# Kernel tuning notes

Hardware: AMD Instinct MI355X
Metric: run time of the kernel (lower is better)

The kernel has to match this reference:

```python
import jax, jax.numpy as jnp
import numpy as np

V, D, H, L, F, MAXLEN = 30522, 768, 12, 12, 3072, 1000
B, S = 16, 512
DH = D // H
SCALE = np.float32(1.0 / np.sqrt(DH))


def setup_inputs() -> dict:
    key = jax.random.key(0)
    ks = jax.random.split(key, 32)
    p = lambda k, shape: (jax.random.normal(k, shape, dtype=jnp.float32) * 0.02)
    inp = {}
    inp["tokens"] = jax.random.randint(ks[0], (B, S), 0, V, dtype=jnp.int32)
    inp["segments"] = jax.random.randint(ks[1], (B, S), 0, 2, dtype=jnp.int32)
    inp["valid_lens"] = jax.random.randint(ks[2], (B,), 64, S + 1, dtype=jnp.int32)
    inp["tok_emb"] = p(ks[3], (V, D))
    inp["seg_emb"] = p(ks[4], (2, D))
    inp["pos_emb"] = jax.random.normal(ks[5], (1, MAXLEN, D), dtype=jnp.float32)
    # stacked per-layer parameters (L leading axis); Linear stored as [in,out]
    inp["Wq"] = p(ks[6], (L, D, D)); inp["bq"] = p(ks[7], (L, D))
    inp["Wk"] = p(ks[8], (L, D, D)); inp["bk"] = p(ks[9], (L, D))
    inp["Wv"] = p(ks[10], (L, D, D)); inp["bv"] = p(ks[11], (L, D))
    inp["Wo"] = p(ks[12], (L, D, D)); inp["bo"] = p(ks[13], (L, D))
    inp["W1"] = p(ks[14], (L, D, F)); inp["b1"] = p(ks[15], (L, F))
    inp["W2"] = p(ks[16], (L, F, D)); inp["b2"] = p(ks[17], (L, D))
    inp["ln1_g"] = jnp.ones((L, D), jnp.float32); inp["ln1_b"] = jnp.zeros((L, D), jnp.float32)
    inp["ln2_g"] = jnp.ones((L, D), jnp.float32); inp["ln2_b"] = jnp.zeros((L, D), jnp.float32)
    return inp


def _layer_norm(x, g, b):
    m = jnp.mean(x, axis=-1, keepdims=True)
    v = jnp.var(x, axis=-1, keepdims=True)
    return (x - m) * jax.lax.rsqrt(v + 1e-5) * g + b


def reference(tokens, segments, valid_lens, tok_emb, seg_emb, pos_emb,
              Wq, bq, Wk, bk, Wv, bv, Wo, bo, W1, b1, W2, b2,
              ln1_g, ln1_b, ln2_g, ln2_b):
    # embeddings + positional add (pos_embedding.data -> no grad, matched via stop_gradient)
    X = tok_emb[tokens] + seg_emb[segments] + jax.lax.stop_gradient(pos_emb)[:, :S, :]
    # key positions >= valid_len are masked (fill -1e6, like the torch code)
    key_mask = jnp.arange(S)[None, :] >= valid_lens[:, None]  # [B,S]

    def blk(X, params):
        wq, bq_, wk, bk_, wv, bv_, wo, bo_, w1, b1_, w2, b2_, g1, be1, g2, be2 = params
        heads = lambda y: y.reshape(B, S, H, DH).transpose(0, 2, 1, 3)  # [B,H,S,DH]
        q = heads(X @ wq + bq_)
        k = heads(X @ wk + bk_)
        v = heads(X @ wv + bv_)
        scores = jnp.einsum('bhqd,bhkd->bhqk', q, k) * SCALE  # [B,H,S,S]
        scores = jnp.where(key_mask[:, None, None, :], jnp.float32(-1e6), scores)
        w = jax.nn.softmax(scores, axis=-1)
        o = jnp.einsum('bhqk,bhkd->bhqd', w, v).transpose(0, 2, 1, 3).reshape(B, S, D)
        X = _layer_norm(X + o @ wo + bo_, g1, be1)
        Y = jax.nn.relu(X @ w1 + b1_) @ w2 + b2_
        X = _layer_norm(X + Y, g2, be2)
        return X, None

    params = (Wq, bq, Wk, bk, Wv, bv, Wo, bo, W1, b1, W2, b2, ln1_g, ln1_b, ln2_g, ln2_b)
    X, _ = jax.lax.scan(blk, X, params)
    return X
```

## Files before the change

### kernel.cpp

```cpp
#include <hip/hip_runtime.h>
#include <hip/hip_bf16.h>

typedef __bf16 bf16_t;
typedef __bf16 bf16x8 __attribute__((ext_vector_type(8)));
typedef float  f32x4  __attribute__((ext_vector_type(4)));

static constexpr int ND = 768;
static constexpr int NH = 12;
static constexpr int NL = 12;
static constexpr int NF = 3072;
static constexpr int NB = 16;
static constexpr int NS = 512;
static constexpr int DH = 64;
static constexpr int MTOK = NB * NS;

#define MFMA_BF16 __builtin_amdgcn_mfma_f32_16x16x32_bf16

__device__ __forceinline__ void gload16(const bf16_t* g, const bf16_t* l) {
    __builtin_amdgcn_global_load_lds(
        (const __attribute__((address_space(1))) void*)(unsigned long long)g,
        (__attribute__((address_space(3))) void*)(unsigned int)(unsigned long long)l,
        16, 0, 0);
}

__global__ __launch_bounds__(256) void embed_kernel(
    const int* __restrict__ tokens, const int* __restrict__ segments,
    const float* __restrict__ tok_emb, const float* __restrict__ seg_emb,
    const float* __restrict__ pos_emb, float* __restrict__ X,
    bf16_t* __restrict__ Xb)
{
    const int t = blockIdx.x;
    const int s = t & (NS - 1);
    const int tok = tokens[t], seg = segments[t];
    const float* te = tok_emb + (size_t)tok * ND;
    const float* se = seg_emb + (size_t)seg * ND;
    const float* pe = pos_emb + (size_t)s * ND;
#pragma unroll
    for (int i = 0; i < 3; ++i) {
        int d = threadIdx.x + i * 256;
        float v = te[d] + se[d] + pe[d];
        X[(size_t)t * ND + d]  = v;
        Xb[(size_t)t * ND + d] = (bf16_t)v;
    }
}

__global__ __launch_bounds__(256) void transpose_kernel(
    const float* __restrict__ src, bf16_t* __restrict__ dst,
    int K, int N, size_t src_stride, size_t dst_stride)
{
    __shared__ float tile[32][33];
    const float* s = src + blockIdx.z * src_stride;
    bf16_t*      d = dst + blockIdx.z * dst_stride;
    const int n0 = blockIdx.x * 32, k0 = blockIdx.y * 32;
#pragma unroll
    for (int i = threadIdx.y; i < 32; i += 8)
        tile[i][threadIdx.x] = s[(size_t)(k0 + i) * N + n0 + threadIdx.x];
    __syncthreads();
#pragma unroll
    for (int i = threadIdx.y; i < 32; i += 8)
        d[(size_t)(n0 + i) * K + k0 + threadIdx.x] = (bf16_t)tile[threadIdx.x][i];
}

__global__ __launch_bounds__(256) void concat_bias_kernel(
    const float* __restrict__ bq, const float* __restrict__ bk,
    const float* __restrict__ bv, float* __restrict__ fb)
{
    int idx = blockIdx.x * 256 + threadIdx.x;
    if (idx >= NL * 2304) return;
    int l = idx / 2304, c = idx % 2304;
    float v = (c < 768) ? bq[l * 768 + c]
            : (c < 1536) ? bk[l * 768 + c - 768] : bv[l * 768 + c - 1536];
    fb[idx] = v;
}

template <int MODE>
__global__ __launch_bounds__(256) void gemm_v3(
    const bf16_t* __restrict__ A, const bf16_t* __restrict__ Bt,
    const float* __restrict__ bias, const float* __restrict__ resid,
    float* __restrict__ outF, bf16_t* __restrict__ o1,
    bf16_t* __restrict__ o2, bf16_t* __restrict__ o3,
    int K, int N, int gridN)
{
    __shared__ __align__(16) bf16_t As[2][128 * 64];
    __shared__ __align__(16) bf16_t Bs[2][128 * 64];
    const int nwg = gridDim.x;
    const int l2 = (blockIdx.x & 7) * (nwg >> 3) + (blockIdx.x >> 3);
    const int m0 = (l2 / gridN) * 128, n0 = (l2 % gridN) * 128;

    const int tid = threadIdx.x, lane = tid & 63, wid = tid >> 6;
    const int wr = (wid >> 1) * 64, wc = (wid & 1) * 64;
    const int fr = lane & 15, g = lane >> 4;
    const int sr = lane >> 3;
    const int ssw = ((lane & 7) ^ sr) * 8;

    f32x4 acc[4][4] = {};
    const int nk = K >> 6;

    auto stage = [&](int buf, int kt) {
        const int k0 = kt << 6;
#pragma unroll
        for (int i = 0; i < 4; ++i) {
            const int lr = wid * 32 + i * 8;
            gload16(A + (size_t)(m0 + lr + sr) * K + k0 + ssw, &As[buf][lr * 64]);
        }
#pragma unroll
        for (int i = 0; i < 4; ++i) {
            const int lr = wid * 32 + i * 8;
            gload16(Bt + (size_t)(n0 + lr + sr) * K + k0 + ssw, &Bs[buf][lr * 64]);
        }
    };

    stage(0, 0);
    for (int kt = 0; kt < nk; ++kt) {
        const int cur = kt & 1;
        if (kt + 1 < nk) {
            stage(cur ^ 1, kt + 1);
            asm volatile("s_waitcnt vmcnt(8)" ::: "memory");
        } else {
            asm volatile("s_waitcnt vmcnt(0)" ::: "memory");
        }
        __builtin_amdgcn_s_barrier();
        asm volatile("" ::: "memory");
#pragma unroll
        for (int kk = 0; kk < 2; ++kk) {
            bf16x8 af[4], bfv[4];
#pragma unroll
            for (int m = 0; m < 4; ++m) {
                const int row = wr + m * 16 + fr;
                af[m] = *(const bf16x8*)(
                    &As[cur][row * 64 + (((kk * 4 + g) ^ (fr & 7)) * 8)]);
            }
#pragma unroll
            for (int n = 0; n < 4; ++n) {
                const int row = wc + n * 16 + fr;
                bfv[n] = *(const bf16x8*)(
                    &Bs[cur][row * 64 + (((kk * 4 + g) ^ (fr & 7)) * 8)]);
            }
            __builtin_amdgcn_s_setprio(1);
#pragma unroll
            for (int m = 0; m < 4; ++m)
#pragma unroll
                for (int n = 0; n < 4; ++n)
                    acc[m][n] = MFMA_BF16(af[m], bfv[n], acc[m][n], 0, 0, 0);
            __builtin_amdgcn_s_setprio(0);
        }
        asm volatile("" ::: "memory");
        __builtin_amdgcn_s_barrier();
    }

    const int rr = (lane >> 4) * 4, cc = lane & 15;
#pragma unroll
    for (int m = 0; m < 4; ++m)
#pragma unroll
        for (int n = 0; n < 4; ++n)
#pragma unroll
            for (int j = 0; j < 4; ++j) {
                const int row = m0 + wr + m * 16 + rr + j;
                const int col = n0 + wc + n * 16 + cc;
                const float v = acc[m][n][j] + bias[col];
                if constexpr (MODE == 2) {
                    const size_t idx = (size_t)row * N + col;
                    outF[idx] = v + resid[idx];
                } else if constexpr (MODE == 3) {
                    o1[(size_t)row * N + col] = (bf16_t)fmaxf(v, 0.0f);
                } else {
                    if (col < 768) {
                        o1[(size_t)row * 768 + col] = (bf16_t)v;
                    } else if (col < 1536) {
                        o2[(size_t)row * 768 + col - 768] = (bf16_t)v;
                    } else {
                        const int c = col - 1536;
                        const int b = row >> 9, s = row & (NS - 1);
                        const int hh = c >> 6, dh = c & (DH - 1);
                        o3[(((size_t)(b * NH + hh)) * DH + dh) * NS + s] = (bf16_t)v;
                    }
                }
            }
}

__global__ __launch_bounds__(256) void attn_kernel(
    const bf16_t* __restrict__ Q, const bf16_t* __restrict__ K,
    const bf16_t* __restrict__ Vt, const int* __restrict__ vlens,
    bf16_t* __restrict__ O)
{
    const int h = blockIdx.x, b = blockIdx.y, qb = blockIdx.z;
    const int wid = threadIdx.x >> 6, lane = threadIdx.x & 63;
    const int q0 = qb * 128 + wid * 32;
    const int vl = vlens[b];
    const int fr = lane & 15, g = lane >> 4, g8 = g * 8;

    __shared__ __align__(16) bf16_t Ks[2][64 * 64];
    __shared__ __align__(16) bf16_t Vs[2][64 * 64];
    __shared__ __align__(16) bf16_t Plds[4][32 * 72];
    bf16_t* pl = Plds[wid];

    const bf16_t* kbase = K + ((size_t)(b * NS) * ND + h * DH);
    const bf16_t* vbase = Vt + ((size_t)(b * NH + h) * DH) * NS;

    bf16x8 qf[2][2];
#pragma unroll
    for (int qg = 0; qg < 2; ++qg) {
        const bf16_t* qptr = Q + ((size_t)(b * NS + q0 + qg * 16 + fr) * ND + h * DH);
        qf[qg][0] = *(const bf16x8*)(qptr + g8);
        qf[qg][1] = *(const bf16x8*)(qptr + 32 + g8);
    }
    asm volatile("s_waitcnt vmcnt(0)" ::: "memory");

    f32x4 acc_o[2][4] = {};
    float mrow[2][4], lrow[2][4];
#pragma unroll
    for (int qg = 0; qg < 2; ++qg)
#pragma unroll
        for (int j = 0; j < 4; ++j) { mrow[qg][j] = -1e30f; lrow[qg][j] = 0.f; }

    auto stage = [&](int buf, int t) {
        const int kv0 = t * 64;
#pragma unroll
        for (int i = 0; i < 2; ++i) {
            const int lr = wid * 16 + i * 8;
            const int r  = lr + (lane >> 3);
            const int ss = ((lane & 7) ^ (r & 7)) * 8;
            gload16(kbase + (size_t)(kv0 + r) * ND + ss, &Ks[buf][lr * 64]);
            gload16(vbase + (size_t)r * NS + kv0 + ss,   &Vs[buf][lr * 64]);
        }
    };

    stage(0, 0);
    for (int t = 0; t < 8; ++t) {
        const int cur = t & 1;
        const int kv0 = t * 64;
        if (t < 7) {
            stage(cur ^ 1, t + 1);
            asm volatile("s_waitcnt vmcnt(4)" ::: "memory");
        } else {
            asm volatile("s_waitcnt vmcnt(0)" ::: "memory");
        }
        __builtin_amdgcn_s_barrier();
        asm volatile("" ::: "memory");

        const bf16_t* ks = Ks[cur];
        const bf16_t* vs = Vs[cur];

        f32x4 sc[2][4];
#pragma unroll
        for (int qg = 0; qg < 2; ++qg)
#pragma unroll
            for (int f = 0; f < 4; ++f) sc[qg][f] = (f32x4){0.f, 0.f, 0.f, 0.f};
#pragma unroll
        for (int f = 0; f < 4; ++f) {
            const int row = f * 16 + fr;
            const bf16_t* kr = ks + row * 64;
            bf16x8 kf0 = *(const bf16x8*)(kr + ((g ^ (row & 7)) * 8));
            bf16x8 kf1 = *(const bf16x8*)(kr + (((g + 4) ^ (row & 7)) * 8));
            sc[0][f] = MFMA_BF16(qf[0][0], kf0, sc[0][f], 0, 0, 0);
            sc[0][f] = MFMA_BF16(qf[0][1], kf1, sc[0][f], 0, 0, 0);
            sc[1][f] = MFMA_BF16(qf[1][0], kf0, sc[1][f], 0, 0, 0);
            sc[1][f] = MFMA_BF16(qf[1][1], kf1, sc[1][f], 0, 0, 0);
        }

#pragma unroll
        for (int qg = 0; qg < 2; ++qg) {
            float sv[16];
#pragma unroll
            for (int f = 0; f < 4; ++f) {
                const int col = kv0 + f * 16 + fr;
                const bool masked = col >= vl;
#pragma unroll
                for (int j = 0; j < 4; ++j)
                    sv[f * 4 + j] = masked ? -1e6f : sc[qg][f][j] * 0.125f;
            }
            float pm[4], rs[4], scl[4];
#pragma unroll
            for (int j = 0; j < 4; ++j)
                pm[j] = fmaxf(fmaxf(sv[j], sv[4 + j]), fmaxf(sv[8 + j], sv[12 + j]));
#pragma unroll
            for (int msk = 1; msk < 16; msk <<= 1)
#pragma unroll
                for (int j = 0; j < 4; ++j) pm[j] = fmaxf(pm[j], __shfl_xor(pm[j], msk));
#pragma unroll
            for (int j = 0; j < 4; ++j) {
                const float mnew = fmaxf(mrow[qg][j], pm[j]);
                scl[j] = __expf(mrow[qg][j] - mnew);
                mrow[qg][j] = mnew;
                rs[j] = 0.f;
            }
#pragma unroll
            for (int f = 0; f < 4; ++f)
#pragma unroll
                for (int j = 0; j < 4; ++j) {
                    const float pv = __expf(sv[f * 4 + j] - mrow[qg][j]);
                    rs[j] += pv;
                    pl[(qg * 16 + g * 4 + j) * 72 + f * 16 + fr] = (bf16_t)pv;
                }
#pragma unroll
            for (int msk = 1; msk < 16; msk <<= 1)
#pragma unroll
                for (int j = 0; j < 4; ++j) rs[j] += __shfl_xor(rs[j], msk);
#pragma unroll
            for (int j = 0; j < 4; ++j) {
                lrow[qg][j] = lrow[qg][j] * scl[j] + rs[j];
#pragma unroll
                for (int n = 0; n < 4; ++n) acc_o[qg][n][j] *= scl[j];
            }
        }

        bf16x8 pf[2][2];
#pragma unroll
        for (int qg = 0; qg < 2; ++qg)
#pragma unroll
            for (int c = 0; c < 2; ++c)
                pf[qg][c] = *(const bf16x8*)(pl + (qg * 16 + fr) * 72 + c * 32 + g8);
#pragma unroll
        for (int n = 0; n < 4; ++n) {
            const int row = n * 16 + fr;
            const bf16_t* vr = vs + row * 64;
            bf16x8 vf0 = *(const bf16x8*)(vr + ((g ^ (row & 7)) * 8));
            bf16x8 vf1 = *(const bf16x8*)(vr + (((g + 4) ^ (row & 7)) * 8));
            acc_o[0][n] = MFMA_BF16(pf[0][0], vf0, acc_o[0][n], 0, 0, 0);
            acc_o[0][n] = MFMA_BF16(pf[0][1], vf1, acc_o[0][n], 0, 0, 0);
            acc_o[1][n] = MFMA_BF16(pf[1][0], vf0, acc_o[1][n], 0, 0, 0);
            acc_o[1][n] = MFMA_BF16(pf[1][1], vf1, acc_o[1][n], 0, 0, 0);
        }

        asm volatile("" ::: "memory");
        __builtin_amdgcn_s_barrier();
    }

#pragma unroll
    for (int qg = 0; qg < 2; ++qg)
#pragma unroll
        for (int n = 0; n < 4; ++n)
#pragma unroll
            for (int j = 0; j < 4; ++j) {
                const int row = q0 + qg * 16 + g * 4 + j;
                O[(size_t)(b * NS + row) * ND + h * DH + n * 16 + fr] =
                    (bf16_t)(acc_o[qg][n][j] / lrow[qg][j]);
            }
}

__global__ __launch_bounds__(256) void ln_kernel(
    const float* __restrict__ Z, const float* __restrict__ g,
    const float* __restrict__ bt, float* __restrict__ X, bf16_t* __restrict__ Xb)
{
    const int t = blockIdx.x;
    const float* z = Z + (size_t)t * ND;
    float x[3];
#pragma unroll
    for (int i = 0; i < 3; ++i) x[i] = z[threadIdx.x + i * 256];
    float s = x[0] + x[1] + x[2];
    float ss = x[0] * x[0] + x[1] * x[1] + x[2] * x[2];
#pragma unroll
    for (int m = 1; m < 64; m <<= 1) {
        s += __shfl_xor(s, m);
        ss += __shfl_xor(ss, m);
    }
    __shared__ float red[8];
    const int wid = threadIdx.x >> 6, lane = threadIdx.x & 63;
    if (lane == 0) { red[wid] = s; red[4 + wid] = ss; }
    __syncthreads();
    s = red[0] + red[1] + red[2] + red[3];
    ss = red[4] + red[5] + red[6] + red[7];
    const float mean = s * (1.0f / ND);
    const float var = ss * (1.0f / ND) - mean * mean;
    const float inv = rsqrtf(var + 1e-5f);
#pragma unroll
    for (int i = 0; i < 3; ++i) {
        int d = threadIdx.x + i * 256;
        float y = (x[i] - mean) * inv * g[d] + bt[d];
        X[(size_t)t * ND + d] = y;
        Xb[(size_t)t * ND + d] = (bf16_t)y;
    }
}

extern "C" void kernel_launch(void* const* d_in, const int* in_sizes, int n_in,
                              void* d_out, int out_size, void* d_ws, size_t ws_size,
                              hipStream_t stream)
{
    (void)in_sizes; (void)n_in; (void)out_size; (void)ws_size;
    const int*   tokens   = (const int*)d_in[0];
    const int*   segments = (const int*)d_in[1];
    const int*   vlens    = (const int*)d_in[2];
    const float* tok_emb  = (const float*)d_in[3];
    const float* seg_emb  = (const float*)d_in[4];
    const float* pos_emb  = (const float*)d_in[5];
    const float* Wq = (const float*)d_in[6];  const float* bq = (const float*)d_in[7];
    const float* Wk = (const float*)d_in[8];  const float* bk = (const float*)d_in[9];
    const float* Wv = (const float*)d_in[10]; const float* bv = (const float*)d_in[11];
    const float* Wo = (const float*)d_in[12]; const float* bo = (const float*)d_in[13];
    const float* W1 = (const float*)d_in[14]; const float* b1 = (const float*)d_in[15];
    const float* W2 = (const float*)d_in[16]; const float* b2 = (const float*)d_in[17];
    const float* g1 = (const float*)d_in[18]; const float* be1 = (const float*)d_in[19];
    const float* g2 = (const float*)d_in[20]; const float* be2 = (const float*)d_in[21];

    float* X = (float*)d_out;

    char* p = (char*)d_ws;
    auto carve = [&](size_t elems, size_t esz) {
        void* r = (void*)p;
        p += (elems * esz + 255) & ~(size_t)255;
        return r;
    };
    bf16_t* wqkvT = (bf16_t*)carve((size_t)NL * 2304 * ND, 2);
    bf16_t* woT   = (bf16_t*)carve((size_t)NL * ND * ND, 2);
    bf16_t* w1T   = (bf16_t*)carve((size_t)NL * NF * ND, 2);
    bf16_t* w2T   = (bf16_t*)carve((size_t)NL * ND * NF, 2);
    float*  fb    = (float*)carve((size_t)NL * 2304, 4);
    bf16_t* Xb    = (bf16_t*)carve((size_t)MTOK * ND, 2);
    bf16_t* Qb    = (bf16_t*)carve((size_t)MTOK * ND, 2);
    bf16_t* Kb    = (bf16_t*)carve((size_t)MTOK * ND, 2);
    bf16_t* Vtb   = (bf16_t*)carve((size_t)MTOK * ND, 2);
    bf16_t* Ob    = (bf16_t*)carve((size_t)MTOK * ND, 2);
    bf16_t* H1    = (bf16_t*)carve((size_t)MTOK * NF, 2);
    float*  Z     = (float*)carve((size_t)MTOK * ND, 4);

    embed_kernel<<<MTOK, 256, 0, stream>>>(tokens, segments, tok_emb, seg_emb,
                                           pos_emb, X, Xb);
    const dim3 tb(32, 8);
    const size_t qkvs = (size_t)2304 * ND;
    transpose_kernel<<<dim3(ND / 32, ND / 32, NL), tb, 0, stream>>>(
        Wq, wqkvT, ND, ND, (size_t)ND * ND, qkvs);
    transpose_kernel<<<dim3(ND / 32, ND / 32, NL), tb, 0, stream>>>(
        Wk, wqkvT + (size_t)768 * ND, ND, ND, (size_t)ND * ND, qkvs);
    transpose_kernel<<<dim3(ND / 32, ND / 32, NL), tb, 0, stream>>>(
        Wv, wqkvT + (size_t)1536 * ND, ND, ND, (size_t)ND * ND, qkvs);
    transpose_kernel<<<dim3(ND / 32, ND / 32, NL), tb, 0, stream>>>(
        Wo, woT, ND, ND, (size_t)ND * ND, (size_t)ND * ND);
    transpose_kernel<<<dim3(NF / 32, ND / 32, NL), tb, 0, stream>>>(
        W1, w1T, ND, NF, (size_t)ND * NF, (size_t)NF * ND);
    transpose_kernel<<<dim3(ND / 32, NF / 32, NL), tb, 0, stream>>>(
        W2, w2T, NF, ND, (size_t)NF * ND, (size_t)ND * NF);
    concat_bias_kernel<<<(NL * 2304 + 255) / 256, 256, 0, stream>>>(bq, bk, bv, fb);

    for (int l = 0; l < NL; ++l) {
        gemm_v3<4><<<18 * 64, 256, 0, stream>>>(
            Xb, wqkvT + (size_t)l * qkvs, fb + (size_t)l * 2304,
            nullptr, nullptr, Qb, Kb, Vtb, ND, 2304, 18);
        attn_kernel<<<dim3(NH, NB, NS / 128), 256, 0, stream>>>(Qb, Kb, Vtb, vlens, Ob);
        gemm_v3<2><<<6 * 64, 256, 0, stream>>>(
            Ob, woT + (size_t)l * ND * ND, bo + l * ND, X, Z,
            nullptr, nullptr, nullptr, ND, ND, 6);
        ln_kernel<<<MTOK, 256, 0, stream>>>(Z, g1 + l * ND, be1 + l * ND, X, Xb);
        gemm_v3<3><<<24 * 64, 256, 0, stream>>>(
            Xb, w1T + (size_t)l * ND * NF, b1 + l * NF, nullptr, nullptr,
            H1, nullptr, nullptr, ND, NF, 24);
        gemm_v3<2><<<6 * 64, 256, 0, stream>>>(
            H1, w2T + (size_t)l * ND * NF, b2 + l * ND, X, Z,
            nullptr, nullptr, nullptr, NF, ND, 6);
        ln_kernel<<<MTOK, 256, 0, stream>>>(Z, g2 + l * ND, be2 + l * ND, X, Xb);
    }
}
```

Baseline: 3.132 ms.

## Use 256x256-tile 8-wave GEMM with phased prefetch for QKV and FFN1

Adds a gemm256 kernel that uses 512 threads (8 waves) and 256x256 output tiles, with each wave computing 128x64. Global-to-LDS prefetch of the next K-tile is split across four sub-phases and interleaved with MFMA work, using per-phase barriers. The aim is more data reuse per LDS byte and better overlap of loads with compute for the QKV and FFN-up GEMMs. The cost is higher register pressure (a 32-fragment accumulator), 128KB of LDS per block, and fewer blocks (288 and 384) in flight on the many CUs. The N=768 GEMMs keep the old 128x128 kernel, now specialized to the residual-output mode.

```diff
diff --git a/kernel.cpp b/kernel.cpp
--- a/kernel.cpp
+++ b/kernel.cpp
@@ -15,6 +15,7 @@
 static constexpr int MTOK = NB * NS;
 
 #define MFMA_BF16 __builtin_amdgcn_mfma_f32_16x16x32_bf16
+#define FENCE() asm volatile("" ::: "memory")
 
 __device__ __forceinline__ void gload16(const bf16_t* g, const bf16_t* l) {
     __builtin_amdgcn_global_load_lds(
@@ -74,94 +75,101 @@
 }
 
 template <int MODE>
-__global__ __launch_bounds__(256) void gemm_v3(
+__global__ __launch_bounds__(512, 2) void gemm256(
     const bf16_t* __restrict__ A, const bf16_t* __restrict__ Bt,
-    const float* __restrict__ bias, const float* __restrict__ resid,
-    float* __restrict__ outF, bf16_t* __restrict__ o1,
-    bf16_t* __restrict__ o2, bf16_t* __restrict__ o3,
+    const float* __restrict__ bias,
+    bf16_t* __restrict__ o1, bf16_t* __restrict__ o2, bf16_t* __restrict__ o3,
     int K, int N, int gridN)
 {
-    __shared__ __align__(16) bf16_t As[2][128 * 64];
-    __shared__ __align__(16) bf16_t Bs[2][128 * 64];
+    __shared__ __align__(16) bf16_t As[2][2][128 * 64];
+    __shared__ __align__(16) bf16_t Bs[2][2][128 * 64];
     const int nwg = gridDim.x;
     const int l2 = (blockIdx.x & 7) * (nwg >> 3) + (blockIdx.x >> 3);
-    const int m0 = (l2 / gridN) * 128, n0 = (l2 % gridN) * 128;
-
+    const int m0 = (l2 / gridN) * 256, n0 = (l2 % gridN) * 256;
     const int tid = threadIdx.x, lane = tid & 63, wid = tid >> 6;
-    const int wr = (wid >> 1) * 64, wc = (wid & 1) * 64;
+    const int wm = wid >> 2, wn = wid & 3;
     const int fr = lane & 15, g = lane >> 4;
-    const int sr = lane >> 3;
-    const int ssw = ((lane & 7) ^ sr) * 8;
-
-    f32x4 acc[4][4] = {};
-    const int nk = K >> 6;
-
-    auto stage = [&](int buf, int kt) {
-        const int k0 = kt << 6;
-#pragma unroll
-        for (int i = 0; i < 4; ++i) {
-            const int lr = wid * 32 + i * 8;
-            gload16(A + (size_t)(m0 + lr + sr) * K + k0 + ssw, &As[buf][lr * 64]);
-        }
-#pragma unroll
-        for (int i = 0; i < 4; ++i) {
-            const int lr = wid * 32 + i * 8;
-            gload16(Bt + (size_t)(n0 + lr + sr) * K + k0 + ssw, &Bs[buf][lr * 64]);
-        }
+    const int sr8 = lane >> 3, sc = lane & 7;
+    const int nt = K >> 6;
+
+    auto stA = [&](int buf, int half, int j, int kt) {
+        const int r = j * 64 + wid * 8 + sr8;
+        gload16(A + (size_t)(m0 + half * 128 + r) * K + (kt << 6) + ((sc ^ sr8) * 8),
+                &As[buf][half][j * 4096 + wid * 512]);
     };
-
-    stage(0, 0);
-    for (int kt = 0; kt < nk; ++kt) {
-        const int cur = kt & 1;
-        if (kt + 1 < nk) {
-            stage(cur ^ 1, kt + 1);
-            asm volatile("s_waitcnt vmcnt(8)" ::: "memory");
-        } else {
-            asm volatile("s_waitcnt vmcnt(0)" ::: "memory");
-        }
-        __builtin_amdgcn_s_barrier();
-        asm volatile("" ::: "memory");
-#pragma unroll
-        for (int kk = 0; kk < 2; ++kk) {
-            bf16x8 af[4], bfv[4];
-#pragma unroll
-            for (int m = 0; m < 4; ++m) {
-                const int row = wr + m * 16 + fr;
-                af[m] = *(const bf16x8*)(
-                    &As[cur][row * 64 + (((kk * 4 + g) ^ (fr & 7)) * 8)]);
-            }
-#pragma unroll
-            for (int n = 0; n < 4; ++n) {
-                const int row = wc + n * 16 + fr;
-                bfv[n] = *(const bf16x8*)(
-                    &Bs[cur][row * 64 + (((kk * 4 + g) ^ (fr & 7)) * 8)]);
-            }
+    auto stB = [&](int buf, int half, int j, int kt) {
+        const int r = j * 64 + wid * 8 + sr8;
+        gload16(Bt + (size_t)(n0 + half * 128 + r) * K + (kt << 6) + ((sc ^ sr8) * 8),
+                &Bs[buf][half][j * 4096 + wid * 512]);
+    };
+
+    stB(0, 0, 0, 0); stB(0, 0, 1, 0); stB(0, 1, 0, 0); stB(0, 1, 1, 0);
+    stA(0, 0, 0, 0); stA(0, 1, 0, 0); stA(0, 0, 1, 0); stA(0, 1, 1, 0);
+    asm volatile("s_waitcnt vmcnt(0)" ::: "memory");
+    FENCE(); __builtin_amdgcn_s_barrier(); FENCE();
+
+    f32x4 acc[8][4] = {};
+    for (int t = 0; t < nt; ++t) {
+        const int buf = t & 1, nb = buf ^ 1;
+        const bf16_t* Ah = &As[buf][wm][0];
+        const bf16_t* Bh = &Bs[buf][wn >> 1][0];
+        const int brow = (wn & 1) * 64;
+        const bool pf = (t + 1 < nt);
+
+        bf16x8 bfr[4][2];
+#pragma unroll
+        for (int nf = 0; nf < 4; ++nf)
+#pragma unroll
+            for (int ks = 0; ks < 2; ++ks)
+                bfr[nf][ks] = *(const bf16x8*)&Bh[(brow + nf * 16 + fr) * 64 +
+                                                  (((ks * 4 + g) ^ (fr & 7)) * 8)];
+#pragma unroll
+        for (int p = 0; p < 4; ++p) {
+            bf16x8 afr[2][2];
+#pragma unroll
+            for (int i = 0; i < 2; ++i)
+#pragma unroll
+                for (int ks = 0; ks < 2; ++ks)
+                    afr[i][ks] = *(const bf16x8*)&Ah[((p * 2 + i) * 16 + fr) * 64 +
+                                                     (((ks * 4 + g) ^ (fr & 7)) * 8)];
+            if (pf) {
+                if (p == 0)      { stB(nb, 0, 0, t + 1); stB(nb, 0, 1, t + 1); }
+                else if (p == 1) { stB(nb, 1, 0, t + 1); stB(nb, 1, 1, t + 1); }
+                else if (p == 2) { stA(nb, 0, 0, t + 1); stA(nb, 1, 0, t + 1); }
+                else             { stA(nb, 0, 1, t + 1); stA(nb, 1, 1, t + 1); }
+            }
+            if (p == 1) {
+                if (pf) asm volatile("s_waitcnt vmcnt(4)" ::: "memory");
+                else    asm volatile("s_waitcnt vmcnt(0)" ::: "memory");
+            }
+            if (p == 3 && pf) asm volatile("s_waitcnt vmcnt(2)" ::: "memory");
+            FENCE(); __builtin_amdgcn_s_barrier(); FENCE();
+            asm volatile("s_waitcnt lgkmcnt(0)" ::: "memory");
             __builtin_amdgcn_s_setprio(1);
 #pragma unroll
-            for (int m = 0; m < 4; ++m)
-#pragma unroll
-                for (int n = 0; n < 4; ++n)
-                    acc[m][n] = MFMA_BF16(af[m], bfv[n], acc[m][n], 0, 0, 0);
+            for (int i = 0; i < 2; ++i)
+#pragma unroll
+                for (int nf = 0; nf < 4; ++nf)
+#pragma unroll
+                    for (int ks = 0; ks < 2; ++ks)
+                        acc[p * 2 + i][nf] =
+                            MFMA_BF16(afr[i][ks], bfr[nf][ks], acc[p * 2 + i][nf], 0, 0, 0);
             __builtin_amdgcn_s_setprio(0);
-        }
-        asm volatile("" ::: "memory");
-        __builtin_amdgcn_s_barrier();
+            FENCE(); __builtin_amdgcn_s_barrier(); FENCE();
+        }
     }
 
     const int rr = (lane >> 4) * 4, cc = lane & 15;
 #pragma unroll
-    for (int m = 0; m < 4; ++m)
-#pragma unroll
-        for (int n = 0; n < 4; ++n)
+    for (int mf = 0; mf < 8; ++mf)
+#pragma unroll
+        for (int nf = 0; nf < 4; ++nf)
 #pragma unroll
             for (int j = 0; j < 4; ++j) {
-                const int row = m0 + wr + m * 16 + rr + j;
-                const int col = n0 + wc + n * 16 + cc;
-                const float v = acc[m][n][j] + bias[col];
-                if constexpr (MODE == 2) {
-                    const size_t idx = (size_t)row * N + col;
-                    outF[idx] = v + resid[idx];
-                } else if constexpr (MODE == 3) {
+                const int row = m0 + wm * 128 + mf * 16 + rr + j;
+                const int col = n0 + wn * 64 + nf * 16 + cc;
+                const float v = acc[mf][nf][j] + bias[col];
+                if constexpr (MODE == 3) {
                     o1[(size_t)row * N + col] = (bf16_t)fmaxf(v, 0.0f);
                 } else {
                     if (col < 768) {
@@ -178,6 +186,92 @@
             }
 }
 
+template <int MODE>
+__global__ __launch_bounds__(256) void gemm_v3(
+    const bf16_t* __restrict__ A, const bf16_t* __restrict__ Bt,
+    const float* __restrict__ bias, const float* __restrict__ resid,
+    float* __restrict__ outF, int K, int N, int gridN)
+{
+    __shared__ __align__(16) bf16_t As[2][128 * 64];
+    __shared__ __align__(16) bf16_t Bs[2][128 * 64];
+    const int nwg = gridDim.x;
+    const int l2 = (blockIdx.x & 7) * (nwg >> 3) + (blockIdx.x >> 3);
+    const int m0 = (l2 / gridN) * 128, n0 = (l2 % gridN) * 128;
+
+    const int tid = threadIdx.x, lane = tid & 63, wid = tid >> 6;
+    const int wr = (wid >> 1) * 64, wc = (wid & 1) * 64;
+    const int fr = lane & 15, g = lane >> 4;
+    const int sr = lane >> 3;
+    const int ssw = ((lane & 7) ^ sr) * 8;
+
+    f32x4 acc[4][4] = {};
+    const int nk = K >> 6;
+
+    auto stage = [&](int buf, int kt) {
+        const int k0 = kt << 6;
+#pragma unroll
+        for (int i = 0; i < 4; ++i) {
+            const int lr = wid * 32 + i * 8;
+            gload16(A + (size_t)(m0 + lr + sr) * K + k0 + ssw, &As[buf][lr * 64]);
+        }
+#pragma unroll
+        for (int i = 0; i < 4; ++i) {
+            const int lr = wid * 32 + i * 8;
+            gload16(Bt + (size_t)(n0 + lr + sr) * K + k0 + ssw, &Bs[buf][lr * 64]);
+        }
+    };
+
+    stage(0, 0);
+    for (int kt = 0; kt < nk; ++kt) {
+        const int cur = kt & 1;
+        if (kt + 1 < nk) {
+            stage(cur ^ 1, kt + 1);
+            asm volatile("s_waitcnt vmcnt(8)" ::: "memory");
+        } else {
+            asm volatile("s_waitcnt vmcnt(0)" ::: "memory");
+        }
+        FENCE(); __builtin_amdgcn_s_barrier(); FENCE();
+#pragma unroll
+        for (int kk = 0; kk < 2; ++kk) {
+            bf16x8 af[4], bfv[4];
+#pragma unroll
+            for (int m = 0; m < 4; ++m) {
+                const int row = wr + m * 16 + fr;
+                af[m] = *(const bf16x8*)(
+                    &As[cur][row * 64 + (((kk * 4 + g) ^ (fr & 7)) * 8)]);
+            }
+#pragma unroll
+            for (int n = 0; n < 4; ++n) {
+                const int row = wc + n * 16 + fr;
+                bfv[n] = *(const bf16x8*)(
+                    &Bs[cur][row * 64 + (((kk * 4 + g) ^ (fr & 7)) * 8)]);
+            }
+            __builtin_amdgcn_s_setprio(1);
+#pragma unroll
+            for (int m = 0; m < 4; ++m)
+#pragma unroll
+                for (int n = 0; n < 4; ++n)
+                    acc[m][n] = MFMA_BF16(af[m], bfv[n], acc[m][n], 0, 0, 0);
+            __builtin_amdgcn_s_setprio(0);
+        }
+        FENCE(); __builtin_amdgcn_s_barrier(); FENCE();
+    }
+
+    const int rr = (lane >> 4) * 4, cc = lane & 15;
+#pragma unroll
+    for (int m = 0; m < 4; ++m)
+#pragma unroll
+        for (int n = 0; n < 4; ++n)
+#pragma unroll
+            for (int j = 0; j < 4; ++j) {
+                const int row = m0 + wr + m * 16 + rr + j;
+                const int col = n0 + wc + n * 16 + cc;
+                const float v = acc[m][n][j] + bias[col];
+                const size_t idx = (size_t)row * N + col;
+                outF[idx] = v + resid[idx];
+            }
+}
+
 __global__ __launch_bounds__(256) void attn_kernel(
     const bf16_t* __restrict__ Q, const bf16_t* __restrict__ K,
     const bf16_t* __restrict__ Vt, const int* __restrict__ vlens,
@@ -235,8 +329,7 @@
         } else {
             asm volatile("s_waitcnt vmcnt(0)" ::: "memory");
         }
-        __builtin_amdgcn_s_barrier();
-        asm volatile("" ::: "memory");
+        FENCE(); __builtin_amdgcn_s_barrier(); FENCE();
 
         const bf16_t* ks = Ks[cur];
         const bf16_t* vs = Vs[cur];
@@ -322,8 +415,7 @@
             acc_o[1][n] = MFMA_BF16(pf[1][1], vf1, acc_o[1][n], 0, 0, 0);
         }
 
-        asm volatile("" ::: "memory");
-        __builtin_amdgcn_s_barrier();
+        FENCE(); __builtin_amdgcn_s_barrier(); FENCE();
     }
 
 #pragma unroll
@@ -432,20 +524,18 @@
     concat_bias_kernel<<<(NL * 2304 + 255) / 256, 256, 0, stream>>>(bq, bk, bv, fb);
 
     for (int l = 0; l < NL; ++l) {
-        gemm_v3<4><<<18 * 64, 256, 0, stream>>>(
+        gemm256<4><<<32 * 9, 512, 0, stream>>>(
             Xb, wqkvT + (size_t)l * qkvs, fb + (size_t)l * 2304,
-            nullptr, nullptr, Qb, Kb, Vtb, ND, 2304, 18);
+            Qb, Kb, Vtb, ND, 2304, 9);
         attn_kernel<<<dim3(NH, NB, NS / 128), 256, 0, stream>>>(Qb, Kb, Vtb, vlens, Ob);
         gemm_v3<2><<<6 * 64, 256, 0, stream>>>(
-            Ob, woT + (size_t)l * ND * ND, bo + l * ND, X, Z,
-            nullptr, nullptr, nullptr, ND, ND, 6);
+            Ob, woT + (size_t)l * ND * ND, bo + l * ND, X, Z, ND, ND, 6);
         ln_kernel<<<MTOK, 256, 0, stream>>>(Z, g1 + l * ND, be1 + l * ND, X, Xb);
-        gemm_v3<3><<<24 * 64, 256, 0, stream>>>(
-            Xb, w1T + (size_t)l * ND * NF, b1 + l * NF, nullptr, nullptr,
-            H1, nullptr, nullptr, ND, NF, 24);
+        gemm256<3><<<32 * 12, 512, 0, stream>>>(
+            Xb, w1T + (size_t)l * ND * NF, b1 + l * NF,
+            H1, nullptr, nullptr, ND, NF, 12);
         gemm_v3<2><<<6 * 64, 256, 0, stream>>>(
-            H1, w2T + (size_t)l * ND * NF, b2 + l * ND, X, Z,
-            nullptr, nullptr, nullptr, NF, ND, 6);
+            H1, w2T + (size_t)l * ND * NF, b2 + l * ND, X, Z, NF, ND, 6);
         ln_kernel<<<MTOK, 256, 0, stream>>>(Z, g2 + l * ND, be2 + l * ND, X, Xb);
     }
 }
```

Result: slower. 3.519 ms (+12.4%).
